# Optimization experiments

Measured on AMD Instinct MI355X. Metric: run time of the kernel, lower is better.

Reference implementation:

```python
import jax, jax.numpy as jnp
import numpy as np

K = 9          # kernel_size
PAD = K // 2   # same padding
SIGMA = 1.0
EPS = 1e-5     # BatchNorm eps


def setup_inputs() -> dict:
    key = jax.random.key(0)
    k0, k1, k2 = jax.random.split(key, 3)
    B, Cin, Cout, L = 4, 64, 64, 131072
    x = jax.random.normal(k0, (B, Cin, L), jnp.float32)
    coords = jax.random.uniform(k1, (B, 3, L), jnp.float32)  # 3D point coords in [0,1)
    W = jax.random.normal(k2, (Cout, Cin, K), jnp.float32) * (1.0 / np.sqrt(Cin * K))
    bias = jnp.zeros((Cout,), jnp.float32)
    gamma = jnp.ones((Cout,), jnp.float32)
    beta = jnp.zeros((Cout,), jnp.float32)
    return {"x": x, "coords": coords, "W": W, "bias": bias, "gamma": gamma, "beta": beta}


def reference(x, coords, W, bias, gamma, beta):
    B, Cin, L = x.shape
    # zero-pad sequence dim for 'same' conv
    xpad = jnp.pad(x, ((0, 0), (0, 0), (PAD, PAD)))
    cpad = jnp.pad(coords, ((0, 0), (0, 0), (PAD, PAD)))
    # unfold: neighbor windows of size K (K is a small compile-time constant)
    x_unf = jnp.stack([xpad[:, :, k:k + L] for k in range(K)], axis=2)   # [B,Cin,K,L]
    c_unf = jnp.stack([cpad[:, :, k:k + L] for k in range(K)], axis=2)   # [B,3,K,L]
    # Gaussian spatial weights from coord distances (WeightedConv1D)
    dist2 = jnp.sum((c_unf - coords[:, :, None, :]) ** 2, axis=1)        # [B,K,L]
    w = jnp.exp(-dist2 / (2.0 * SIGMA * SIGMA))                          # [B,K,L]
    # weighted conv: contract over (Cin, K)
    out = jnp.einsum('ock,bckl->bol', W, x_unf * w[:, None, :, :])       # [B,Cout,L]
    out = out + bias[None, :, None]
    # BatchNorm1d (training-mode batch statistics over B and L) + ReLU
    mean = out.mean(axis=(0, 2), keepdims=True)
    var = out.var(axis=(0, 2), keepdims=True)
    out = (out - mean) * jax.lax.rsqrt(var + EPS)
    out = out * gamma[None, :, None] + beta[None, :, None]
    return jax.nn.relu(out)
```

## Files before the change

### kernel.cpp

```cpp
#include <hip/hip_runtime.h>
#include <hip/hip_bf16.h>

#define KK 9
#define PADK 4
#define CIN 64
#define COUT 64
#define LSEQ 131072
#define NB 4
#define TILE 64
#define XROWS 72
#define XRS 72
#define NTILES 2048
#define NPART 64

typedef __attribute__((ext_vector_type(8))) short v8s;
typedef __attribute__((ext_vector_type(4))) float v4f;

__device__ __forceinline__ unsigned short f2bf(float f) {
  __hip_bfloat16 h = __float2bfloat16(f);
  return *reinterpret_cast<unsigned short*>(&h);
}
__device__ __forceinline__ float bf2f(unsigned short s) {
  return __uint_as_float(((unsigned)s) << 16);
}

__device__ __forceinline__ void store_o(float* p, float v) { *p = v; }
__device__ __forceinline__ void store_o(__hip_bfloat16* p, float v) { *p = __float2bfloat16(v); }

__global__ void wtrans_kernel(const float* __restrict__ W, v8s* __restrict__ Wt) {
  int t = blockIdx.x * 256 + threadIdx.x;
  if (t >= KK * 2 * 4 * 64) return;
  int lane = t & 63;
  int frag = t >> 6;
  int mblk = frag & 3;
  int s    = (frag >> 2) & 1;
  int k    = frag >> 3;
  int m = lane & 15, q = lane >> 4;
  int o = mblk * 16 + m;
  union { v8s v; unsigned short h[8]; } u;
#pragma unroll
  for (int j = 0; j < 8; ++j) {
    int c = 32 * s + q * 8 + j;
    u.h[j] = f2bf(W[(o * CIN + c) * KK + k]);
  }
  Wt[t] = u.v;
}

template <typename OutT>
__global__ __launch_bounds__(256, 2)
void conv_kernel(const float* __restrict__ x, const float* __restrict__ coords,
                 const v8s* __restrict__ Wt, OutT* __restrict__ cv,
                 float* __restrict__ stat_sum, float* __restrict__ stat_sq) {
  __shared__ __align__(16) __hip_bfloat16 xt[4][XROWS][XRS];
  __shared__ float wt[4][KK][TILE];
  __shared__ float ct[4][3][XROWS];

  const int wv   = threadIdx.x >> 6;
  const int lane = threadIdx.x & 63;
  const int gw   = blockIdx.x * 4 + wv;
  const int b    = gw >> 11;
  const int tile = gw & (NTILES - 1);
  const int l0   = tile * TILE;
  const float* xb = x + (b * CIN) * LSEQ;
  const float* cb = coords + (b * 3) * LSEQ;
  const int m = lane & 15;
  const int q = lane >> 4;

  {
#pragma unroll
    for (int rep = 0; rep < 8; ++rep) {
      int p = q + 4 * rep;
      int c = 2 * p;
      const float* s0 = xb + c * LSEQ + l0 + 4 * m;
      float4 a0 = *(const float4*)(s0);
      float4 a1 = *(const float4*)(s0 + LSEQ);
      float e0[4] = {a0.x, a0.y, a0.z, a0.w};
      float e1[4] = {a1.x, a1.y, a1.z, a1.w};
#pragma unroll
      for (int j = 0; j < 4; ++j) {
        unsigned pk = ((unsigned)f2bf(e1[j]) << 16) | (unsigned)f2bf(e0[j]);
        *(unsigned*)&xt[wv][4 + 4 * m + j][c] = pk;
      }
    }
  }
  {
    int c = lane;
    float el[4] = {0.f, 0.f, 0.f, 0.f};
    float er[4] = {0.f, 0.f, 0.f, 0.f};
    if (tile != 0) {
#pragma unroll
      for (int j = 0; j < 4; ++j) el[j] = xb[c * LSEQ + l0 - 4 + j];
    }
    if (tile != NTILES - 1) {
#pragma unroll
      for (int j = 0; j < 4; ++j) er[j] = xb[c * LSEQ + l0 + TILE + j];
    }
#pragma unroll
    for (int j = 0; j < 4; ++j) {
      xt[wv][j][c]      = __float2bfloat16(el[j]);
      xt[wv][68 + j][c] = __float2bfloat16(er[j]);
    }
  }
  {
#pragma unroll
    for (int d = 0; d < 3; ++d) {
      for (int r = lane; r < XROWS; r += 64) {
        int l = l0 - PADK + r;
        float v = 0.f;
        if (l >= 0 && l < LSEQ) v = cb[d * LSEQ + l];
        ct[wv][d][r] = v;
      }
    }
  }
  __syncthreads();

  {
    float cx = ct[wv][0][lane + PADK];
    float cy = ct[wv][1][lane + PADK];
    float cz = ct[wv][2][lane + PADK];
#pragma unroll
    for (int k = 0; k < KK; ++k) {
      float dx = ct[wv][0][lane + k] - cx;
      float dy = ct[wv][1][lane + k] - cy;
      float dz = ct[wv][2][lane + k] - cz;
      wt[wv][k][lane] = __expf(-0.5f * (dx * dx + dy * dy + dz * dz));
    }
  }
  __syncthreads();

  v4f acc[4][4];
#pragma unroll
  for (int i = 0; i < 4; ++i)
#pragma unroll
    for (int j = 0; j < 4; ++j)
      acc[i][j] = (v4f){0.f, 0.f, 0.f, 0.f};

#pragma unroll 1
  for (int k = 0; k < KK; ++k) {
    v8s afr[2][4];
#pragma unroll
    for (int s = 0; s < 2; ++s)
#pragma unroll
      for (int mb = 0; mb < 4; ++mb)
        afr[s][mb] = Wt[((k * 2 + s) * 4 + mb) * 64 + lane];
#pragma unroll
    for (int nb = 0; nb < 4; ++nb) {
      float wsc = wt[wv][k][nb * 16 + m];
      const __hip_bfloat16* rowp = &xt[wv][nb * 16 + m + k][0];
#pragma unroll
      for (int s = 0; s < 2; ++s) {
        union { v8s v; unsigned u[4]; } bi, bo;
        bi.v = *(const v8s*)(rowp + q * 8 + 32 * s);
#pragma unroll
        for (int i = 0; i < 4; ++i) {
          float lo = __uint_as_float(bi.u[i] << 16) * wsc;
          float hi = __uint_as_float(bi.u[i] & 0xffff0000u) * wsc;
          bo.u[i] = ((unsigned)f2bf(hi) << 16) | (unsigned)f2bf(lo);
        }
#pragma unroll
        for (int mb = 0; mb < 4; ++mb)
          acc[mb][nb] = __builtin_amdgcn_mfma_f32_16x16x32_bf16(
              afr[s][mb], bo.v, acc[mb][nb], 0, 0, 0);
      }
    }
  }

  const int part = gw & (NPART - 1);
  OutT* outb = cv + (b * COUT) * LSEQ;
#pragma unroll
  for (int mb = 0; mb < 4; ++mb) {
#pragma unroll
    for (int r = 0; r < 4; ++r) {
      int o = mb * 16 + q * 4 + r;
      float s1 = 0.f, s2 = 0.f;
#pragma unroll
      for (int nb = 0; nb < 4; ++nb) {
        float v = acc[mb][nb][r];
        s1 += v;
        s2 += v * v;
        store_o(&outb[o * LSEQ + l0 + nb * 16 + m], v);
      }
#pragma unroll
      for (int off = 1; off < 16; off <<= 1) {
        s1 += __shfl_xor(s1, off, 64);
        s2 += __shfl_xor(s2, off, 64);
      }
      if (m == 0) {
        atomicAdd(&stat_sum[part * COUT + o], s1);
        atomicAdd(&stat_sq [part * COUT + o], s2);
      }
    }
  }
}

__global__ void finalize_kernel(const float* __restrict__ stat_sum,
                                const float* __restrict__ stat_sq,
                                const float* __restrict__ gamma,
                                const float* __restrict__ beta,
                                float* __restrict__ ss) {
  int o = threadIdx.x;
  float s1 = 0.f, s2 = 0.f;
  for (int p = 0; p < NPART; ++p) {
    s1 += stat_sum[p * COUT + o];
    s2 += stat_sq [p * COUT + o];
  }
  const float invN = 1.0f / (float)(NB * LSEQ);
  float mean = s1 * invN;
  float var  = s2 * invN - mean * mean;
  float sc = gamma[o] * rsqrtf(var + 1e-5f);
  ss[o]        = sc;
  ss[COUT + o] = beta[o] - mean * sc;
}

__global__ __launch_bounds__(256)
void scale_f32_kernel(float* __restrict__ data, const float* __restrict__ ss) {
  const int blk = blockIdx.x;
  const int ch = (blk >> 6) & 63;
  const float sc = ss[ch];
  const float sh = ss[COUT + ch];
  const int base = blk * 2048 + threadIdx.x * 8;
  float4 a = *(float4*)(data + base);
  float4 b = *(float4*)(data + base + 4);
  a.x = fmaxf(fmaf(a.x, sc, sh), 0.f);
  a.y = fmaxf(fmaf(a.y, sc, sh), 0.f);
  a.z = fmaxf(fmaf(a.z, sc, sh), 0.f);
  a.w = fmaxf(fmaf(a.w, sc, sh), 0.f);
  b.x = fmaxf(fmaf(b.x, sc, sh), 0.f);
  b.y = fmaxf(fmaf(b.y, sc, sh), 0.f);
  b.z = fmaxf(fmaf(b.z, sc, sh), 0.f);
  b.w = fmaxf(fmaf(b.w, sc, sh), 0.f);
  *(float4*)(data + base)     = a;
  *(float4*)(data + base + 4) = b;
}

__global__ __launch_bounds__(256)
void scale_bf16_kernel(const __hip_bfloat16* __restrict__ cvin,
                       const float* __restrict__ ss, float* __restrict__ out) {
  const int blk = blockIdx.x;
  const int ch = (blk >> 6) & 63;
  const float sc = ss[ch];
  const float sh = ss[COUT + ch];
  const int base = blk * 2048 + threadIdx.x * 8;
  union { v8s v; unsigned short h[8]; } u;
  u.v = *(const v8s*)(cvin + base);
  float r[8];
#pragma unroll
  for (int i = 0; i < 8; ++i)
    r[i] = fmaxf(fmaf(bf2f(u.h[i]), sc, sh), 0.f);
  *(float4*)(out + base)     = make_float4(r[0], r[1], r[2], r[3]);
  *(float4*)(out + base + 4) = make_float4(r[4], r[5], r[6], r[7]);
}

extern "C" void kernel_launch(void* const* d_in, const int* in_sizes, int n_in,
                              void* d_out, int out_size, void* d_ws, size_t ws_size,
                              hipStream_t stream) {
  const float* x      = (const float*)d_in[0];
  const float* coords = (const float*)d_in[1];
  const float* W      = (const float*)d_in[2];
  const float* gamma  = (const float*)d_in[4];
  const float* beta   = (const float*)d_in[5];
  float* out = (float*)d_out;
  char* ws = (char*)d_ws;

  float* stat_sum = (float*)(ws);
  float* stat_sq  = (float*)(ws + 16384);
  float* ss       = (float*)(ws + 32768);
  v8s*   Wt       = (v8s*)(ws + 40960);
  __hip_bfloat16* scratch = (__hip_bfloat16*)(ws + 131072);

  const size_t need_bf16 = (size_t)131072 + (size_t)NB * COUT * LSEQ * 2;
  const bool bf16_path = ws_size >= need_bf16;

  hipMemsetAsync(ws, 0, 32768, stream);
  wtrans_kernel<<<18, 256, 0, stream>>>(W, Wt);

  if (bf16_path) {
    conv_kernel<__hip_bfloat16><<<NB * NTILES / 4, 256, 0, stream>>>(
        x, coords, Wt, scratch, stat_sum, stat_sq);
    finalize_kernel<<<1, COUT, 0, stream>>>(stat_sum, stat_sq, gamma, beta, ss);
    scale_bf16_kernel<<<(NB * COUT * (LSEQ / 2048)), 256, 0, stream>>>(scratch, ss, out);
  } else {
    conv_kernel<float><<<NB * NTILES / 4, 256, 0, stream>>>(
        x, coords, Wt, out, stat_sum, stat_sq);
    finalize_kernel<<<1, COUT, 0, stream>>>(stat_sum, stat_sq, gamma, beta, ss);
    scale_f32_kernel<<<(NB * COUT * (LSEQ / 2048)), 256, 0, stream>>>(out, ss);
  }
}
```

Before: 338.6 us.

## Apply Gaussian weights post-MFMA via telescoping differences; one wave per block

```diff
diff --git a/kernel.cpp b/kernel.cpp
--- a/kernel.cpp
+++ b/kernel.cpp
@@ -47,17 +47,15 @@
 }
 
 template <typename OutT>
-__global__ __launch_bounds__(256, 2)
+__global__ __launch_bounds__(64, 3)
 void conv_kernel(const float* __restrict__ x, const float* __restrict__ coords,
                  const v8s* __restrict__ Wt, OutT* __restrict__ cv,
                  float* __restrict__ stat_sum, float* __restrict__ stat_sq) {
-  __shared__ __align__(16) __hip_bfloat16 xt[4][XROWS][XRS];
-  __shared__ float wt[4][KK][TILE];
-  __shared__ float ct[4][3][XROWS];
-
-  const int wv   = threadIdx.x >> 6;
+  __shared__ __align__(16) __hip_bfloat16 xt[XROWS][XRS];
+  __shared__ float wt[KK][TILE];
+
   const int lane = threadIdx.x & 63;
-  const int gw   = blockIdx.x * 4 + wv;
+  const int gw   = blockIdx.x;
   const int b    = gw >> 11;
   const int tile = gw & (NTILES - 1);
   const int l0   = tile * TILE;
@@ -66,21 +64,20 @@
   const int m = lane & 15;
   const int q = lane >> 4;
 
-  {
-#pragma unroll
-    for (int rep = 0; rep < 8; ++rep) {
-      int p = q + 4 * rep;
-      int c = 2 * p;
-      const float* s0 = xb + c * LSEQ + l0 + 4 * m;
-      float4 a0 = *(const float4*)(s0);
-      float4 a1 = *(const float4*)(s0 + LSEQ);
-      float e0[4] = {a0.x, a0.y, a0.z, a0.w};
-      float e1[4] = {a1.x, a1.y, a1.z, a1.w};
-#pragma unroll
-      for (int j = 0; j < 4; ++j) {
-        unsigned pk = ((unsigned)f2bf(e1[j]) << 16) | (unsigned)f2bf(e0[j]);
-        *(unsigned*)&xt[wv][4 + 4 * m + j][c] = pk;
-      }
+#pragma unroll
+  for (int rep = 0; rep < 2; ++rep) {
+    int cg = 8 * (q + 4 * rep);
+    float4 f[8];
+#pragma unroll
+    for (int t = 0; t < 8; ++t)
+      f[t] = *(const float4*)(xb + (cg + t) * LSEQ + l0 + 4 * m);
+    const float* fp = (const float*)&f[0];
+#pragma unroll
+    for (int j = 0; j < 4; ++j) {
+      union { v8s v; unsigned short h[8]; } u;
+#pragma unroll
+      for (int t = 0; t < 8; ++t) u.h[t] = f2bf(fp[4 * t + j]);
+      *(v8s*)&xt[4 + 4 * m + j][cg] = u.v;
     }
   }
   {
@@ -97,71 +94,67 @@
     }
 #pragma unroll
     for (int j = 0; j < 4; ++j) {
-      xt[wv][j][c]      = __float2bfloat16(el[j]);
-      xt[wv][68 + j][c] = __float2bfloat16(er[j]);
+      xt[j][c]      = __float2bfloat16(el[j]);
+      xt[68 + j][c] = __float2bfloat16(er[j]);
     }
   }
   {
-#pragma unroll
-    for (int d = 0; d < 3; ++d) {
-      for (int r = lane; r < XROWS; r += 64) {
-        int l = l0 - PADK + r;
-        float v = 0.f;
-        if (l >= 0 && l < LSEQ) v = cb[d * LSEQ + l];
-        ct[wv][d][r] = v;
-      }
-    }
+    int n = lane;
+    float sx = cb[l0 + n];
+    float sy = cb[LSEQ + l0 + n];
+    float sz = cb[2 * LSEQ + l0 + n];
+    float w9[KK];
+#pragma unroll
+    for (int k = 0; k < KK; ++k) {
+      int l = l0 + n + k - PADK;
+      float cx = 0.f, cy = 0.f, cz = 0.f;
+      if ((unsigned)l < (unsigned)LSEQ) {
+        cx = cb[l]; cy = cb[LSEQ + l]; cz = cb[2 * LSEQ + l];
+      }
+      float dx = cx - sx, dy = cy - sy, dz = cz - sz;
+      w9[k] = __expf(-0.5f * (dx * dx + dy * dy + dz * dz));
+    }
+#pragma unroll
+    for (int k = 0; k < KK; ++k)
+      wt[k][n] = w9[k] - ((k < KK - 1) ? w9[k + 1] : 0.f);
   }
   __syncthreads();
 
-  {
-    float cx = ct[wv][0][lane + PADK];
-    float cy = ct[wv][1][lane + PADK];
-    float cz = ct[wv][2][lane + PADK];
-#pragma unroll
-    for (int k = 0; k < KK; ++k) {
-      float dx = ct[wv][0][lane + k] - cx;
-      float dy = ct[wv][1][lane + k] - cy;
-      float dz = ct[wv][2][lane + k] - cz;
-      wt[wv][k][lane] = __expf(-0.5f * (dx * dx + dy * dy + dz * dz));
-    }
-  }
-  __syncthreads();
-
-  v4f acc[4][4];
+  v4f y[4][4], tot[4][4];
 #pragma unroll
   for (int i = 0; i < 4; ++i)
 #pragma unroll
-    for (int j = 0; j < 4; ++j)
-      acc[i][j] = (v4f){0.f, 0.f, 0.f, 0.f};
+    for (int j = 0; j < 4; ++j) {
+      y[i][j]   = (v4f){0.f, 0.f, 0.f, 0.f};
+      tot[i][j] = (v4f){0.f, 0.f, 0.f, 0.f};
+    }
 
 #pragma unroll 1
   for (int k = 0; k < KK; ++k) {
-    v8s afr[2][4];
-#pragma unroll
-    for (int s = 0; s < 2; ++s)
+    const v8s* wk = Wt + k * 512;
+#pragma unroll
+    for (int s = 0; s < 2; ++s) {
+      v8s a0 = wk[(s * 4 + 0) * 64 + lane];
+      v8s a1 = wk[(s * 4 + 1) * 64 + lane];
+      v8s a2 = wk[(s * 4 + 2) * 64 + lane];
+      v8s a3 = wk[(s * 4 + 3) * 64 + lane];
+#pragma unroll
+      for (int nb = 0; nb < 4; ++nb) {
+        v8s bf = *(const v8s*)&xt[nb * 16 + m + k][q * 8 + 32 * s];
+        y[0][nb] = __builtin_amdgcn_mfma_f32_16x16x32_bf16(a0, bf, y[0][nb], 0, 0, 0);
+        y[1][nb] = __builtin_amdgcn_mfma_f32_16x16x32_bf16(a1, bf, y[1][nb], 0, 0, 0);
+        y[2][nb] = __builtin_amdgcn_mfma_f32_16x16x32_bf16(a2, bf, y[2][nb], 0, 0, 0);
+        y[3][nb] = __builtin_amdgcn_mfma_f32_16x16x32_bf16(a3, bf, y[3][nb], 0, 0, 0);
+      }
+    }
+#pragma unroll
+    for (int nb = 0; nb < 4; ++nb) {
+      float d = wt[k][nb * 16 + m];
 #pragma unroll
       for (int mb = 0; mb < 4; ++mb)
-        afr[s][mb] = Wt[((k * 2 + s) * 4 + mb) * 64 + lane];
-#pragma unroll
-    for (int nb = 0; nb < 4; ++nb) {
-      float wsc = wt[wv][k][nb * 16 + m];
-      const __hip_bfloat16* rowp = &xt[wv][nb * 16 + m + k][0];
-#pragma unroll
-      for (int s = 0; s < 2; ++s) {
-        union { v8s v; unsigned u[4]; } bi, bo;
-        bi.v = *(const v8s*)(rowp + q * 8 + 32 * s);
-#pragma unroll
-        for (int i = 0; i < 4; ++i) {
-          float lo = __uint_as_float(bi.u[i] << 16) * wsc;
-          float hi = __uint_as_float(bi.u[i] & 0xffff0000u) * wsc;
-          bo.u[i] = ((unsigned)f2bf(hi) << 16) | (unsigned)f2bf(lo);
-        }
-#pragma unroll
-        for (int mb = 0; mb < 4; ++mb)
-          acc[mb][nb] = __builtin_amdgcn_mfma_f32_16x16x32_bf16(
-              afr[s][mb], bo.v, acc[mb][nb], 0, 0, 0);
-      }
+#pragma unroll
+        for (int r = 0; r < 4; ++r)
+          tot[mb][nb][r] = __builtin_fmaf(d, y[mb][nb][r], tot[mb][nb][r]);
     }
   }
 
@@ -175,7 +168,7 @@
       float s1 = 0.f, s2 = 0.f;
 #pragma unroll
       for (int nb = 0; nb < 4; ++nb) {
-        float v = acc[mb][nb][r];
+        float v = tot[mb][nb][r];
         s1 += v;
         s2 += v * v;
         store_o(&outb[o * LSEQ + l0 + nb * 16 + m], v);
@@ -275,12 +268,12 @@
   wtrans_kernel<<<18, 256, 0, stream>>>(W, Wt);
 
   if (bf16_path) {
-    conv_kernel<__hip_bfloat16><<<NB * NTILES / 4, 256, 0, stream>>>(
+    conv_kernel<__hip_bfloat16><<<NB * NTILES, 64, 0, stream>>>(
         x, coords, Wt, scratch, stat_sum, stat_sq);
     finalize_kernel<<<1, COUT, 0, stream>>>(stat_sum, stat_sq, gamma, beta, ss);
     scale_bf16_kernel<<<(NB * COUT * (LSEQ / 2048)), 256, 0, stream>>>(scratch, ss, out);
   } else {
-    conv_kernel<float><<<NB * NTILES / 4, 256, 0, stream>>>(
+    conv_kernel<float><<<NB * NTILES, 64, 0, stream>>>(
         x, coords, Wt, out, stat_sum, stat_sq);
     finalize_kernel<<<1, COUT, 0, stream>>>(stat_sum, stat_sq, gamma, beta, ss);
     scale_f32_kernel<<<(NB * COUT * (LSEQ / 2048)), 256, 0, stream>>>(out, ss);
```

After: 328.5 us. 3.0% less time.
